# Performance work log

Measured on AMD Instinct MI355X. Metric: run time of the kernel, lower is better.

## Reference

```python
import jax, jax.numpy as jnp
import numpy as np

N = 100000
E = 1600000
IN_CH, HID_CH, OUT_CH, HEADS = 128, 32, 64, 4
NEG_SLOPE = 0.2


def gat_conv(x, src, dst, W, att_src, att_dst, bias, concat):
    """PyG-style GATConv (inference; dropout off). src/dst include self-loops.
    x: [N, Fin], W: [Fin, H*C], att_*: [H, C], bias: [H*C] or [C]."""
    n = x.shape[0]
    H, C = att_src.shape
    h = (x @ W).reshape(n, H, C)                      # [N, H, C]
    a_s = jnp.sum(h * att_src, axis=-1)               # [N, H]
    a_d = jnp.sum(h * att_dst, axis=-1)               # [N, H]
    e = jax.nn.leaky_relu(a_s[src] + a_d[dst], NEG_SLOPE)   # [E, H]
    # segment softmax over incoming edges of each dst node
    e_max = jax.ops.segment_max(e, dst, num_segments=n)     # [N, H]
    e_exp = jnp.exp(e - e_max[dst])                          # [E, H]
    denom = jax.ops.segment_sum(e_exp, dst, num_segments=n) # [N, H]
    alpha = e_exp / (denom[dst] + 1e-16)                     # [E, H]
    msg = h[src] * alpha[:, :, None]                         # [E, H, C]
    out = jax.ops.segment_sum(msg, dst, num_segments=n)     # [N, H, C]
    out = out.reshape(n, H * C) if concat else out.mean(axis=1)
    return out + bias


def setup_inputs() -> dict:
    key = jax.random.key(0)
    ks = jax.random.split(key, 10)
    g = 1.0 / np.sqrt(IN_CH)
    g2 = 1.0 / np.sqrt(HID_CH * HEADS)
    return {
        "x": jax.random.normal(ks[0], (N, IN_CH), dtype=jnp.float32),
        "edge_index": jax.random.randint(ks[1], (2, E), 0, N, dtype=jnp.int64),
        "W1": jax.random.normal(ks[2], (IN_CH, HEADS * HID_CH), dtype=jnp.float32) * g,
        "att_src1": jax.random.normal(ks[3], (HEADS, HID_CH), dtype=jnp.float32) * g,
        "att_dst1": jax.random.normal(ks[4], (HEADS, HID_CH), dtype=jnp.float32) * g,
        "b1": jnp.zeros((HEADS * HID_CH,), dtype=jnp.float32),
        "W2": jax.random.normal(ks[5], (HEADS * HID_CH, OUT_CH), dtype=jnp.float32) * g2,
        "att_src2": jax.random.normal(ks[6], (1, OUT_CH), dtype=jnp.float32) * g2,
        "att_dst2": jax.random.normal(ks[7], (1, OUT_CH), dtype=jnp.float32) * g2,
        "b2": jnp.zeros((OUT_CH,), dtype=jnp.float32),
    }


def reference(x, edge_index, W1, att_src1, att_dst1, b1, W2, att_src2, att_dst2, b2):
    n = x.shape[0]
    # GATConv adds self-loops by default (fixed-size concat: jit friendly)
    loops = jnp.arange(n, dtype=edge_index.dtype)
    src = jnp.concatenate([edge_index[0], loops])
    dst = jnp.concatenate([edge_index[1], loops])
    h = gat_conv(x, src, dst, W1, att_src1, att_dst1, b1, concat=True)
    h = jax.nn.elu(h)
    return gat_conv(h, src, dst, W2, att_src2, att_dst2, b2, concat=False)
```

## Files before the change

kernel.cpp:

```cpp
#include <hip/hip_runtime.h>
#include <hip/hip_fp16.h>

#define NEG_SLOPE 0.2f
#define BKN 128
#define MAXNB 1024
#define GRP 256

typedef _Float16 half_t;
typedef __attribute__((ext_vector_type(8))) _Float16 half8;
typedef __attribute__((ext_vector_type(4))) float floatx4;

__global__ __launch_bounds__(256) void w_convert(
    const float* __restrict__ W, half_t* __restrict__ Wt, int N)
{
    int i = blockIdx.x * 256 + threadIdx.x;
    if (i >= 128 * N) return;
    int k = i / N, nn = i % N;
    Wt[nn * 128 + k] = (half_t)W[i];
}

template<int BN, int HEADS>
__global__ __launch_bounds__(256) void gemm_mfma(
    const float* __restrict__ X, const half_t* __restrict__ Wt,
    const float* __restrict__ atts, const float* __restrict__ attd,
    half_t* __restrict__ H, float* __restrict__ As, float* __restrict__ Ad,
    int n)
{
    constexpr int K  = 128;
    constexpr int NT = BN / 16;
    constexpr int TPH = NT / HEADS;

    __shared__ half_t Wl[BN * K];
    __shared__ half_t Xl[64 * K];

    const int t = threadIdx.x;
    const int wave = t >> 6, lane = t & 63;
    const int quad = lane >> 4, c = lane & 15;

    float att_s[NT], att_d[NT];
    #pragma unroll
    for (int nt = 0; nt < NT; ++nt) {
        att_s[nt] = atts[nt * 16 + c];
        att_d[nt] = attd[nt * 16 + c];
    }

    for (int i = t; i < BN * 16; i += 256) {
        int row = i >> 4, cid = i & 15;
        half8 v = *(const half8*)(Wt + row * K + cid * 8);
        *(half8*)(Wl + row * K + ((cid ^ (row & 15)) << 3)) = v;
    }

    const int numTiles = (n + 63) / 64;
    for (int tile = blockIdx.x; tile < numTiles; tile += gridDim.x) {
        const int row0 = tile * 64;
        __syncthreads();
        for (int i = t; i < 1024; i += 256) {
            int m = i >> 4, cid = i & 15;
            int row = row0 + m;
            float4 a = make_float4(0.f,0.f,0.f,0.f), b = a;
            if (row < n) {
                const float4* src = (const float4*)(X + (size_t)row * K + cid * 8);
                a = src[0]; b = src[1];
            }
            half8 h;
            h[0]=(half_t)a.x; h[1]=(half_t)a.y; h[2]=(half_t)a.z; h[3]=(half_t)a.w;
            h[4]=(half_t)b.x; h[5]=(half_t)b.y; h[6]=(half_t)b.z; h[7]=(half_t)b.w;
            *(half8*)(Xl + m * K + ((cid ^ (m & 15)) << 3)) = h;
        }
        __syncthreads();

        floatx4 acc[NT];
        #pragma unroll
        for (int i = 0; i < NT; ++i) acc[i] = (floatx4)(0.f);

        #pragma unroll
        for (int kc = 0; kc < 4; ++kc) {
            int cid = kc * 4 + quad;
            half8 afrag = *(const half8*)(Xl + (wave * 16 + c) * K + ((cid ^ c) << 3));
            #pragma unroll
            for (int nt = 0; nt < NT; ++nt) {
                half8 bfrag = *(const half8*)(Wl + (nt * 16 + c) * K + ((cid ^ c) << 3));
                acc[nt] = __builtin_amdgcn_mfma_f32_16x16x32_f16(afrag, bfrag, acc[nt], 0, 0, 0);
            }
        }

        #pragma unroll
        for (int reg = 0; reg < 4; ++reg) {
            int row = row0 + wave * 16 + quad * 4 + reg;
            bool ok = row < n;
            if (ok) {
                #pragma unroll
                for (int nt = 0; nt < NT; ++nt)
                    H[(size_t)row * BN + nt * 16 + c] = (half_t)acc[nt][reg];
            }
            #pragma unroll
            for (int h = 0; h < HEADS; ++h) {
                float ps = 0.f, pd = 0.f;
                #pragma unroll
                for (int u = 0; u < TPH; ++u) {
                    int nt = h * TPH + u;
                    ps += acc[nt][reg] * att_s[nt];
                    pd += acc[nt][reg] * att_d[nt];
                }
                #pragma unroll
                for (int off = 1; off < 16; off <<= 1) {
                    ps += __shfl_xor(ps, off);
                    pd += __shfl_xor(pd, off);
                }
                if (ok && c == 0) {
                    As[(size_t)row * HEADS + h] = ps;
                    Ad[(size_t)row * HEADS + h] = pd;
                }
            }
        }
    }
}

__global__ __launch_bounds__(256) void ghist(
    const int* __restrict__ ei, int E, int Etot, int NB, int chunk,
    int* __restrict__ cnt)
{
    __shared__ int h[MAXNB];
    int g = blockIdx.x;
    for (int i = threadIdx.x; i < NB; i += 256) h[i] = 0;
    __syncthreads();
    int lo = g * chunk, hi = min(Etot, lo + chunk);
    for (int e = lo + threadIdx.x; e < hi; e += 256) {
        int dst = (e < E) ? ei[E + e] : (e - E);
        atomicAdd(&h[dst >> 7], 1);
    }
    __syncthreads();
    for (int i = threadIdx.x; i < NB; i += 256) cnt[i * GRP + g] = h[i];
}

__global__ __launch_bounds__(256) void scan_blocks(
    int* __restrict__ data, int n, int* __restrict__ bsum)
{
    __shared__ int s[256];
    int t = threadIdx.x;
    int idx = blockIdx.x * 1024 + t * 4;
    int4 v = make_int4(0, 0, 0, 0);
    if (idx + 3 < n)      v = *(const int4*)(data + idx);
    else {
        if (idx     < n) v.x = data[idx];
        if (idx + 1 < n) v.y = data[idx+1];
        if (idx + 2 < n) v.z = data[idx+2];
        if (idx + 3 < n) v.w = data[idx+3];
    }
    int tsum = v.x + v.y + v.z + v.w;
    s[t] = tsum;
    __syncthreads();
    for (int off = 1; off < 256; off <<= 1) {
        int x = (t >= off) ? s[t - off] : 0;
        __syncthreads();
        s[t] += x;
        __syncthreads();
    }
    int excl = s[t] - tsum;
    if (t == 255) bsum[blockIdx.x] = s[255];
    if (idx     < n) data[idx]     = excl;
    if (idx + 1 < n) data[idx + 1] = excl + v.x;
    if (idx + 2 < n) data[idx + 2] = excl + v.x + v.y;
    if (idx + 3 < n) data[idx + 3] = excl + v.x + v.y + v.z;
}

__global__ __launch_bounds__(256) void scan_sums(int* __restrict__ bsum, int nb)
{
    __shared__ int s[256];
    int t = threadIdx.x;
    int v = (t < nb) ? bsum[t] : 0;
    s[t] = v;
    __syncthreads();
    for (int off = 1; off < 256; off <<= 1) {
        int x = (t >= off) ? s[t - off] : 0;
        __syncthreads();
        s[t] += x;
        __syncthreads();
    }
    if (t < nb) bsum[t] = s[t] - v;
}

__global__ __launch_bounds__(256) void scan_add(
    int* __restrict__ data, int n, const int* __restrict__ bsum)
{
    int i = blockIdx.x * 256 + threadIdx.x;
    if (i < n) data[i] += bsum[i >> 10];
}

__global__ __launch_bounds__(256) void pass1_scatter(
    const int* __restrict__ ei, int E, int Etot, int NB, int chunk,
    const int* __restrict__ S, unsigned* __restrict__ tmp)
{
    __shared__ int cur[MAXNB];
    int g = blockIdx.x;
    for (int i = threadIdx.x; i < NB; i += 256) cur[i] = S[i * GRP + g];
    __syncthreads();
    int lo = g * chunk, hi = min(Etot, lo + chunk);
    for (int e = lo + threadIdx.x; e < hi; e += 256) {
        int src, dst;
        if (e < E) { src = ei[e]; dst = ei[E + e]; }
        else       { src = dst = e - E; }
        int pos = atomicAdd(&cur[dst >> 7], 1);
        tmp[pos] = ((unsigned)src << 7) | (unsigned)(dst & (BKN - 1));
    }
}

__global__ __launch_bounds__(256) void pass2_sort(
    const unsigned* __restrict__ tmp, const int* __restrict__ S,
    int NB, int Etot,
    int* __restrict__ offs, int* __restrict__ esrc, int n)
{
    __shared__ int cnt[BKN];
    __shared__ int sc[BKN];
    __shared__ int cur[BKN];
    int bk = blockIdx.x;
    int t  = threadIdx.x;
    if (t < BKN) cnt[t] = 0;
    __syncthreads();
    int lo = S[bk * GRP];
    int hi = (bk + 1 < NB) ? S[(bk + 1) * GRP] : Etot;
    for (int i = lo + t; i < hi; i += 256)
        atomicAdd(&cnt[tmp[i] & (BKN - 1)], 1);
    __syncthreads();
    int v = (t < BKN) ? cnt[t] : 0;
    if (t < BKN) sc[t] = v;
    __syncthreads();
    for (int off = 1; off < BKN; off <<= 1) {
        int x = (t < BKN && t >= off) ? sc[t - off] : 0;
        __syncthreads();
        if (t < BKN) sc[t] += x;
        __syncthreads();
    }
    if (t < BKN) {
        int node = bk * BKN + t;
        if (node < n) offs[node] = lo + sc[t];
        cur[t] = lo + sc[t] - v;
    }
    __syncthreads();
    for (int i = lo + t; i < hi; i += 256) {
        unsigned w = tmp[i];
        int p = atomicAdd(&cur[w & (BKN - 1)], 1);
        esrc[p] = (int)(w >> 7);
    }
}

__global__ __launch_bounds__(256) void agg1(
    const int* __restrict__ offs, const int* __restrict__ esrc,
    const __half2* __restrict__ Hh, const float* __restrict__ As,
    const float* __restrict__ Ad, const float* __restrict__ bias,
    float* __restrict__ X2, int n)
{
    int v    = (blockIdx.x * 256 + threadIdx.x) >> 6;
    int lane = threadIdx.x & 63;
    if (v >= n) return;
    int end = offs[v];
    int beg = v ? offs[v - 1] : 0;
    int head = lane >> 4;
    float adv = Ad[(size_t)v * 4 + head];
    float accx = 0.f, accy = 0.f, den = 0.f;
    int j = beg;
    for (; j + 3 < end; j += 4) {
        int s0 = esrc[j], s1 = esrc[j+1], s2 = esrc[j+2], s3 = esrc[j+3];
        float e0 = As[(size_t)s0*4 + head] + adv;
        float e1 = As[(size_t)s1*4 + head] + adv;
        float e2 = As[(size_t)s2*4 + head] + adv;
        float e3 = As[(size_t)s3*4 + head] + adv;
        __half2 q0 = Hh[(size_t)s0*64 + lane];
        __half2 q1 = Hh[(size_t)s1*64 + lane];
        __half2 q2 = Hh[(size_t)s2*64 + lane];
        __half2 q3 = Hh[(size_t)s3*64 + lane];
        e0 = e0 > 0.f ? e0 : NEG_SLOPE*e0;  float w0 = __expf(e0);
        e1 = e1 > 0.f ? e1 : NEG_SLOPE*e1;  float w1 = __expf(e1);
        e2 = e2 > 0.f ? e2 : NEG_SLOPE*e2;  float w2 = __expf(e2);
        e3 = e3 > 0.f ? e3 : NEG_SLOPE*e3;  float w3 = __expf(e3);
        float2 f0 = __half22float2(q0);
        float2 f1 = __half22float2(q1);
        float2 f2 = __half22float2(q2);
        float2 f3 = __half22float2(q3);
        accx += w0*f0.x + w1*f1.x + w2*f2.x + w3*f3.x;
        accy += w0*f0.y + w1*f1.y + w2*f2.y + w3*f3.y;
        den  += w0 + w1 + w2 + w3;
    }
    for (; j < end; ++j) {
        int s = esrc[j];
        float e = As[(size_t)s*4 + head] + adv;
        e = e > 0.f ? e : NEG_SLOPE*e;
        float w = __expf(e);
        float2 f = __half22float2(Hh[(size_t)s*64 + lane]);
        accx += w*f.x; accy += w*f.y; den += w;
    }
    float inv = 1.f / (den + 1e-16f);
    float2 b = ((const float2*)bias)[lane];
    float ox = accx*inv + b.x, oy = accy*inv + b.y;
    ox = ox > 0.f ? ox : __expf(ox) - 1.f;
    oy = oy > 0.f ? oy : __expf(oy) - 1.f;
    ((float2*)(X2 + (size_t)v * 128))[lane] = make_float2(ox, oy);
}

__global__ __launch_bounds__(256) void agg2(
    const int* __restrict__ offs, const int* __restrict__ esrc,
    const __half2* __restrict__ Hh, const float* __restrict__ As,
    const float* __restrict__ Ad, const float* __restrict__ bias,
    float* __restrict__ out, int n)
{
    int v    = (blockIdx.x * 256 + threadIdx.x) >> 6;
    int lane = threadIdx.x & 63;
    if (v >= n) return;
    int half = lane >> 5;
    int li   = lane & 31;
    int end = offs[v];
    int beg = v ? offs[v - 1] : 0;
    float adv = Ad[v];
    float accx = 0.f, accy = 0.f, den = 0.f;
    int j = beg + half;
    for (; j + 6 < end; j += 8) {
        int s0 = esrc[j], s1 = esrc[j+2], s2 = esrc[j+4], s3 = esrc[j+6];
        float e0 = As[s0] + adv;
        float e1 = As[s1] + adv;
        float e2 = As[s2] + adv;
        float e3 = As[s3] + adv;
        __half2 q0 = Hh[(size_t)s0*32 + li];
        __half2 q1 = Hh[(size_t)s1*32 + li];
        __half2 q2 = Hh[(size_t)s2*32 + li];
        __half2 q3 = Hh[(size_t)s3*32 + li];
        e0 = e0 > 0.f ? e0 : NEG_SLOPE*e0;  float w0 = __expf(e0);
        e1 = e1 > 0.f ? e1 : NEG_SLOPE*e1;  float w1 = __expf(e1);
        e2 = e2 > 0.f ? e2 : NEG_SLOPE*e2;  float w2 = __expf(e2);
        e3 = e3 > 0.f ? e3 : NEG_SLOPE*e3;  float w3 = __expf(e3);
        float2 f0 = __half22float2(q0);
        float2 f1 = __half22float2(q1);
        float2 f2 = __half22float2(q2);
        float2 f3 = __half22float2(q3);
        accx += w0*f0.x + w1*f1.x + w2*f2.x + w3*f3.x;
        accy += w0*f0.y + w1*f1.y + w2*f2.y + w3*f3.y;
        den  += w0 + w1 + w2 + w3;
    }
    for (; j < end; j += 2) {
        int s = esrc[j];
        float e = As[s] + adv;
        e = e > 0.f ? e : NEG_SLOPE*e;
        float w = __expf(e);
        float2 f = __half22float2(Hh[(size_t)s*32 + li]);
        accx += w*f.x; accy += w*f.y; den += w;
    }
    accx += __shfl_xor(accx, 32);
    accy += __shfl_xor(accy, 32);
    den  += __shfl_xor(den, 32);
    if (half == 0) {
        float inv = 1.f / (den + 1e-16f);
        float2 b = ((const float2*)bias)[li];
        ((float2*)(out + (size_t)v * 64))[li] =
            make_float2(accx*inv + b.x, accy*inv + b.y);
    }
}

extern "C" void kernel_launch(void* const* d_in, const int* in_sizes, int n_in,
                              void* d_out, int out_size, void* d_ws, size_t ws_size,
                              hipStream_t stream)
{
    (void)n_in; (void)out_size; (void)ws_size;
    const float* x   = (const float*)d_in[0];
    const int*   ei  = (const int*)  d_in[1];
    const float* W1  = (const float*)d_in[2];
    const float* as1 = (const float*)d_in[3];
    const float* ad1 = (const float*)d_in[4];
    const float* b1  = (const float*)d_in[5];
    const float* W2  = (const float*)d_in[6];
    const float* as2 = (const float*)d_in[7];
    const float* ad2 = (const float*)d_in[8];
    const float* b2  = (const float*)d_in[9];
    float* out = (float*)d_out;

    const int n    = in_sizes[0] / 128;
    const int E    = in_sizes[1] / 2;
    const int Etot = E + n;
    const int NB   = (n + BKN - 1) / BKN;
    const int chunk = (Etot + GRP - 1) / GRP;

    char* p = (char*)d_ws;
    half_t* Hh = (half_t*)p;  p += (size_t)n * 128 * sizeof(half_t);
    float* X2  = (float*)p;   p += (size_t)n * 128 * sizeof(float);
    float* As1 = (float*)p;   p += (size_t)n * 4 * sizeof(float);
    float* Ad1 = (float*)p;   p += (size_t)n * 4 * sizeof(float);
    int* offs  = (int*)p;     p += (size_t)n * sizeof(int);
    int* esrc  = (int*)p;     p += (size_t)Etot * sizeof(int);
    unsigned* tmp = (unsigned*)p; p += (size_t)Etot * sizeof(unsigned);
    int* cnt   = (int*)p;     p += (size_t)NB * GRP * sizeof(int);
    int* bsum  = (int*)p;     p += 256 * sizeof(int);
    half_t* Wt1 = (half_t*)p; p += 128 * 128 * sizeof(half_t);
    half_t* Wt2 = (half_t*)p; p += 64 * 128 * sizeof(half_t);

    const int scan_n  = NB * GRP;
    const int scan_nb = (scan_n + 1023) / 1024;

    w_convert<<<(128 * 128 + 255) / 256, 256, 0, stream>>>(W1, Wt1, 128);
    w_convert<<<(128 * 64  + 255) / 256, 256, 0, stream>>>(W2, Wt2, 64);

    ghist<<<GRP, 256, 0, stream>>>(ei, E, Etot, NB, chunk, cnt);
    scan_blocks<<<scan_nb, 256, 0, stream>>>(cnt, scan_n, bsum);
    scan_sums<<<1, 256, 0, stream>>>(bsum, scan_nb);
    scan_add<<<(scan_n + 255) / 256, 256, 0, stream>>>(cnt, scan_n, bsum);
    pass1_scatter<<<GRP, 256, 0, stream>>>(ei, E, Etot, NB, chunk, cnt, tmp);
    pass2_sort<<<NB, 256, 0, stream>>>(tmp, cnt, NB, Etot, offs, esrc, n);

    const int gtiles = (n + 63) / 64;

    gemm_mfma<128, 4><<<gtiles, 256, 0, stream>>>(x, Wt1, as1, ad1, Hh, As1, Ad1, n);
    agg1<<<(n * 64 + 255) / 256, 256, 0, stream>>>(offs, esrc, (const __half2*)Hh, As1, Ad1, b1, X2, n);

    gemm_mfma<64, 1><<<gtiles, 256, 0, stream>>>(X2, Wt2, as2, ad2, Hh, As1, Ad1, n);
    agg2<<<(n * 64 + 255) / 256, 256, 0, stream>>>(offs, esrc, (const __half2*)Hh, As1, Ad1, b2, out, n);
}
```

Baseline: 339.8 us.

## Precompute per-edge attention weights in sort pass and vectorize aggregation loads

```diff
diff --git a/kernel.cpp b/kernel.cpp
--- a/kernel.cpp
+++ b/kernel.cpp
@@ -7,6 +7,7 @@
 #define GRP 256
 
 typedef _Float16 half_t;
+typedef __attribute__((ext_vector_type(4))) _Float16 half4;
 typedef __attribute__((ext_vector_type(8))) _Float16 half8;
 typedef __attribute__((ext_vector_type(4))) float floatx4;
 
@@ -208,14 +209,21 @@
 __global__ __launch_bounds__(256) void pass2_sort(
     const unsigned* __restrict__ tmp, const int* __restrict__ S,
     int NB, int Etot,
-    int* __restrict__ offs, int* __restrict__ esrc, int n)
+    const float* __restrict__ As1, const float* __restrict__ Ad1,
+    int* __restrict__ offs, int* __restrict__ esrc,
+    unsigned char* __restrict__ ldst, half_t* __restrict__ w1, int n)
 {
     __shared__ int cnt[BKN];
     __shared__ int sc[BKN];
     __shared__ int cur[BKN];
+    __shared__ float Adl[BKN * 4];
     int bk = blockIdx.x;
     int t  = threadIdx.x;
     if (t < BKN) cnt[t] = 0;
+    for (int i = t; i < BKN * 4; i += 256) {
+        int idx = bk * BKN * 4 + i;
+        Adl[i] = (idx < n * 4) ? Ad1[idx] : 0.f;
+    }
     __syncthreads();
     int lo = S[bk * GRP];
     int hi = (bk + 1 < NB) ? S[(bk + 1) * GRP] : Etot;
@@ -239,55 +247,86 @@
     __syncthreads();
     for (int i = lo + t; i < hi; i += 256) {
         unsigned w = tmp[i];
-        int p = atomicAdd(&cur[w & (BKN - 1)], 1);
-        esrc[p] = (int)(w >> 7);
+        int local = (int)(w & (BKN - 1));
+        int src   = (int)(w >> 7);
+        int p = atomicAdd(&cur[local], 1);
+        esrc[p] = src;
+        ldst[p] = (unsigned char)local;
+        float4 a4 = *(const float4*)(As1 + 4 * src);
+        #pragma unroll
+        for (int h = 0; h < 4; ++h) {
+            float e = ((const float*)&a4)[h] + Adl[local * 4 + h];
+            e = e > 0.f ? e : NEG_SLOPE * e;
+            w1[(size_t)h * Etot + p] = (half_t)__expf(e);
+        }
+    }
+}
+
+__global__ __launch_bounds__(256) void weights2(
+    const int* __restrict__ esrc, const unsigned char* __restrict__ ldst,
+    const int* __restrict__ offs,
+    const float* __restrict__ As2, const float* __restrict__ Ad2,
+    half_t* __restrict__ w2, int NB, int Etot, int n)
+{
+    __shared__ float Adl[BKN];
+    int bk = blockIdx.x;
+    int t  = threadIdx.x;
+    if (t < BKN) {
+        int node = bk * BKN + t;
+        Adl[t] = (node < n) ? Ad2[node] : 0.f;
+    }
+    __syncthreads();
+    int lo = bk ? offs[bk * BKN - 1] : 0;
+    int last = min(bk * BKN + BKN - 1, n - 1);
+    int hi = offs[last];
+    for (int j = lo + t; j < hi; j += 256) {
+        float e = As2[esrc[j]] + Adl[ldst[j]];
+        e = e > 0.f ? e : NEG_SLOPE * e;
+        w2[j] = (half_t)__expf(e);
     }
 }
 
 __global__ __launch_bounds__(256) void agg1(
     const int* __restrict__ offs, const int* __restrict__ esrc,
-    const __half2* __restrict__ Hh, const float* __restrict__ As,
-    const float* __restrict__ Ad, const float* __restrict__ bias,
-    float* __restrict__ X2, int n)
+    const half_t* __restrict__ w1, const __half2* __restrict__ Hh,
+    const float* __restrict__ bias, float* __restrict__ X2, int n, int Etot)
 {
     int v    = (blockIdx.x * 256 + threadIdx.x) >> 6;
     int lane = threadIdx.x & 63;
     if (v >= n) return;
     int end = offs[v];
     int beg = v ? offs[v - 1] : 0;
-    int head = lane >> 4;
-    float adv = Ad[(size_t)v * 4 + head];
+    const half_t* wh = w1 + (size_t)(lane >> 4) * Etot;
     float accx = 0.f, accy = 0.f, den = 0.f;
     int j = beg;
+    for (; j < end && (j & 3); ++j) {
+        int s = esrc[j];
+        float w = (float)wh[j];
+        float2 f = __half22float2(Hh[(unsigned)s * 64 + lane]);
+        accx += w * f.x; accy += w * f.y; den += w;
+    }
     for (; j + 3 < end; j += 4) {
-        int s0 = esrc[j], s1 = esrc[j+1], s2 = esrc[j+2], s3 = esrc[j+3];
-        float e0 = As[(size_t)s0*4 + head] + adv;
-        float e1 = As[(size_t)s1*4 + head] + adv;
-        float e2 = As[(size_t)s2*4 + head] + adv;
-        float e3 = As[(size_t)s3*4 + head] + adv;
-        __half2 q0 = Hh[(size_t)s0*64 + lane];
-        __half2 q1 = Hh[(size_t)s1*64 + lane];
-        __half2 q2 = Hh[(size_t)s2*64 + lane];
-        __half2 q3 = Hh[(size_t)s3*64 + lane];
-        e0 = e0 > 0.f ? e0 : NEG_SLOPE*e0;  float w0 = __expf(e0);
-        e1 = e1 > 0.f ? e1 : NEG_SLOPE*e1;  float w1 = __expf(e1);
-        e2 = e2 > 0.f ? e2 : NEG_SLOPE*e2;  float w2 = __expf(e2);
-        e3 = e3 > 0.f ? e3 : NEG_SLOPE*e3;  float w3 = __expf(e3);
+        int4 s = *(const int4*)(esrc + j);
+        half4 wv = *(const half4*)(wh + j);
+        __half2 q0 = Hh[(unsigned)s.x * 64 + lane];
+        __half2 q1 = Hh[(unsigned)s.y * 64 + lane];
+        __half2 q2 = Hh[(unsigned)s.z * 64 + lane];
+        __half2 q3 = Hh[(unsigned)s.w * 64 + lane];
+        float w0 = (float)wv[0], w1f = (float)wv[1];
+        float w2f = (float)wv[2], w3 = (float)wv[3];
         float2 f0 = __half22float2(q0);
         float2 f1 = __half22float2(q1);
         float2 f2 = __half22float2(q2);
         float2 f3 = __half22float2(q3);
-        accx += w0*f0.x + w1*f1.x + w2*f2.x + w3*f3.x;
-        accy += w0*f0.y + w1*f1.y + w2*f2.y + w3*f3.y;
-        den  += w0 + w1 + w2 + w3;
+        accx += w0*f0.x + w1f*f1.x + w2f*f2.x + w3*f3.x;
+        accy += w0*f0.y + w1f*f1.y + w2f*f2.y + w3*f3.y;
+        den  += w0 + w1f + w2f + w3;
     }
     for (; j < end; ++j) {
         int s = esrc[j];
-        float e = As[(size_t)s*4 + head] + adv;
-        e = e > 0.f ? e : NEG_SLOPE*e;
-        float w = __expf(e);
-        float2 f = __half22float2(Hh[(size_t)s*64 + lane]);
-        accx += w*f.x; accy += w*f.y; den += w;
+        float w = (float)wh[j];
+        float2 f = __half22float2(Hh[(unsigned)s * 64 + lane]);
+        accx += w * f.x; accy += w * f.y; den += w;
     }
     float inv = 1.f / (den + 1e-16f);
     float2 b = ((const float2*)bias)[lane];
@@ -299,9 +338,8 @@
 
 __global__ __launch_bounds__(256) void agg2(
     const int* __restrict__ offs, const int* __restrict__ esrc,
-    const __half2* __restrict__ Hh, const float* __restrict__ As,
-    const float* __restrict__ Ad, const float* __restrict__ bias,
-    float* __restrict__ out, int n)
+    const half_t* __restrict__ w2, const __half2* __restrict__ Hh,
+    const float* __restrict__ bias, float* __restrict__ out, int n)
 {
     int v    = (blockIdx.x * 256 + threadIdx.x) >> 6;
     int lane = threadIdx.x & 63;
@@ -310,38 +348,38 @@
     int li   = lane & 31;
     int end = offs[v];
     int beg = v ? offs[v - 1] : 0;
-    float adv = Ad[v];
     float accx = 0.f, accy = 0.f, den = 0.f;
-    int j = beg + half;
-    for (; j + 6 < end; j += 8) {
-        int s0 = esrc[j], s1 = esrc[j+2], s2 = esrc[j+4], s3 = esrc[j+6];
-        float e0 = As[s0] + adv;
-        float e1 = As[s1] + adv;
-        float e2 = As[s2] + adv;
-        float e3 = As[s3] + adv;
-        __half2 q0 = Hh[(size_t)s0*32 + li];
-        __half2 q1 = Hh[(size_t)s1*32 + li];
-        __half2 q2 = Hh[(size_t)s2*32 + li];
-        __half2 q3 = Hh[(size_t)s3*32 + li];
-        e0 = e0 > 0.f ? e0 : NEG_SLOPE*e0;  float w0 = __expf(e0);
-        e1 = e1 > 0.f ? e1 : NEG_SLOPE*e1;  float w1 = __expf(e1);
-        e2 = e2 > 0.f ? e2 : NEG_SLOPE*e2;  float w2 = __expf(e2);
-        e3 = e3 > 0.f ? e3 : NEG_SLOPE*e3;  float w3 = __expf(e3);
+    int alignEnd = min(end, (beg + 7) & ~7);
+    for (int j = beg + half; j < alignEnd; j += 2) {
+        int s = esrc[j];
+        float w = (float)w2[j];
+        float2 f = __half22float2(Hh[(unsigned)s * 32 + li]);
+        accx += w * f.x; accy += w * f.y; den += w;
+    }
+    int p = alignEnd;
+    for (; p + 7 < end; p += 8) {
+        int jb = p + half * 4;
+        int4 s = *(const int4*)(esrc + jb);
+        half4 wv = *(const half4*)(w2 + jb);
+        __half2 q0 = Hh[(unsigned)s.x * 32 + li];
+        __half2 q1 = Hh[(unsigned)s.y * 32 + li];
+        __half2 q2 = Hh[(unsigned)s.z * 32 + li];
+        __half2 q3 = Hh[(unsigned)s.w * 32 + li];
+        float w0 = (float)wv[0], w1f = (float)wv[1];
+        float w2f = (float)wv[2], w3 = (float)wv[3];
         float2 f0 = __half22float2(q0);
         float2 f1 = __half22float2(q1);
         float2 f2 = __half22float2(q2);
         float2 f3 = __half22float2(q3);
-        accx += w0*f0.x + w1*f1.x + w2*f2.x + w3*f3.x;
-        accy += w0*f0.y + w1*f1.y + w2*f2.y + w3*f3.y;
-        den  += w0 + w1 + w2 + w3;
-    }
-    for (; j < end; j += 2) {
+        accx += w0*f0.x + w1f*f1.x + w2f*f2.x + w3*f3.x;
+        accy += w0*f0.y + w1f*f1.y + w2f*f2.y + w3*f3.y;
+        den  += w0 + w1f + w2f + w3;
+    }
+    for (int j = p + half; j < end; j += 2) {
         int s = esrc[j];
-        float e = As[s] + adv;
-        e = e > 0.f ? e : NEG_SLOPE*e;
-        float w = __expf(e);
-        float2 f = __half22float2(Hh[(size_t)s*32 + li]);
-        accx += w*f.x; accy += w*f.y; den += w;
+        float w = (float)w2[j];
+        float2 f = __half22float2(Hh[(unsigned)s * 32 + li]);
+        accx += w * f.x; accy += w * f.y; den += w;
     }
     accx += __shfl_xor(accx, 32);
     accy += __shfl_xor(accy, 32);
@@ -384,30 +422,37 @@
     float* Ad1 = (float*)p;   p += (size_t)n * 4 * sizeof(float);
     int* offs  = (int*)p;     p += (size_t)n * sizeof(int);
     int* esrc  = (int*)p;     p += (size_t)Etot * sizeof(int);
-    unsigned* tmp = (unsigned*)p; p += (size_t)Etot * sizeof(unsigned);
     int* cnt   = (int*)p;     p += (size_t)NB * GRP * sizeof(int);
-    int* bsum  = (int*)p;     p += 256 * sizeof(int);
+    int* bsum  = (int*)p;     p += 1024;
     half_t* Wt1 = (half_t*)p; p += 128 * 128 * sizeof(half_t);
     half_t* Wt2 = (half_t*)p; p += 64 * 128 * sizeof(half_t);
+    half_t* w1 = (half_t*)p;  p += (size_t)4 * Etot * sizeof(half_t);
+    unsigned char* ldst = (unsigned char*)p;
+    unsigned* tmp = (unsigned*)X2;
+    half_t* w2 = w1;
 
     const int scan_n  = NB * GRP;
     const int scan_nb = (scan_n + 1023) / 1024;
 
     w_convert<<<(128 * 128 + 255) / 256, 256, 0, stream>>>(W1, Wt1, 128);
     w_convert<<<(128 * 64  + 255) / 256, 256, 0, stream>>>(W2, Wt2, 64);
+
+    const int gtiles = (n + 63) / 64;
+    gemm_mfma<128, 4><<<gtiles, 256, 0, stream>>>(x, Wt1, as1, ad1, Hh, As1, Ad1, n);
 
     ghist<<<GRP, 256, 0, stream>>>(ei, E, Etot, NB, chunk, cnt);
     scan_blocks<<<scan_nb, 256, 0, stream>>>(cnt, scan_n, bsum);
     scan_sums<<<1, 256, 0, stream>>>(bsum, scan_nb);
     scan_add<<<(scan_n + 255) / 256, 256, 0, stream>>>(cnt, scan_n, bsum);
     pass1_scatter<<<GRP, 256, 0, stream>>>(ei, E, Etot, NB, chunk, cnt, tmp);
-    pass2_sort<<<NB, 256, 0, stream>>>(tmp, cnt, NB, Etot, offs, esrc, n);
-
-    const int gtiles = (n + 63) / 64;
-
-    gemm_mfma<128, 4><<<gtiles, 256, 0, stream>>>(x, Wt1, as1, ad1, Hh, As1, Ad1, n);
-    agg1<<<(n * 64 + 255) / 256, 256, 0, stream>>>(offs, esrc, (const __half2*)Hh, As1, Ad1, b1, X2, n);
+    pass2_sort<<<NB, 256, 0, stream>>>(tmp, cnt, NB, Etot, As1, Ad1,
+                                       offs, esrc, ldst, w1, n);
+
+    agg1<<<(n * 64 + 255) / 256, 256, 0, stream>>>(offs, esrc, w1,
+        (const __half2*)Hh, b1, X2, n, Etot);
 
     gemm_mfma<64, 1><<<gtiles, 256, 0, stream>>>(X2, Wt2, as2, ad2, Hh, As1, Ad1, n);
-    agg2<<<(n * 64 + 255) / 256, 256, 0, stream>>>(offs, esrc, (const __half2*)Hh, As1, Ad1, b2, out, n);
-}
+    weights2<<<NB, 256, 0, stream>>>(esrc, ldst, offs, As1, Ad1, w2, NB, Etot, n);
+    agg2<<<(n * 64 + 255) / 256, 256, 0, stream>>>(offs, esrc, w2,
+        (const __half2*)Hh, b2, out, n);
+}
```

After: 412.1 us. 1.21x slower.
